# Performance work log

Measured on AMD Instinct MI355X. Metric: run time of the kernel, lower is better.

## Reference

```python
import jax, jax.numpy as jnp
import numpy as np

N_LAYER = 4
N_HEAD = 12
D_MODEL = 768
SEQ_LEN = 2048
VOCAB = 50257
BATCH = 2


def _sinusoid_pe(seq_len, d_model):
    pos = np.arange(seq_len, dtype=np.float32)[:, None]
    div = np.exp(np.arange(0, d_model, 2, dtype=np.float32) * (-np.log(10000.0) / d_model))
    pe = np.zeros((seq_len, d_model), dtype=np.float32)
    pe[:, 0::2] = np.sin(pos * div)
    pe[:, 1::2] = np.cos(pos * div)
    return jnp.asarray(pe[None])  # [1, C, D]


def setup_inputs() -> dict:
    key = jax.random.key(0)
    ks = jax.random.split(key, 12)
    s = 0.02
    return {
        "features": jax.random.randint(ks[0], (BATCH, SEQ_LEN), 0, VOCAB),
        "targets": jax.random.randint(ks[1], (BATCH, SEQ_LEN), 0, VOCAB),
        "tok_embed": jax.random.normal(ks[2], (VOCAB, D_MODEL), jnp.float32) * s,
        "pos_emb": _sinusoid_pe(SEQ_LEN, D_MODEL),
        "ln1_w": jnp.ones((N_LAYER, D_MODEL), jnp.float32),
        "ln1_b": jnp.zeros((N_LAYER, D_MODEL), jnp.float32),
        "attn_w": jax.random.normal(ks[3], (N_LAYER, D_MODEL, 3 * D_MODEL), jnp.float32) * s,
        "attn_b": jnp.zeros((N_LAYER, 3 * D_MODEL), jnp.float32),
        "proj_w": jax.random.normal(ks[4], (N_LAYER, D_MODEL, D_MODEL), jnp.float32) * s,
        "proj_b": jnp.zeros((N_LAYER, D_MODEL), jnp.float32),
        "ln2_w": jnp.ones((N_LAYER, D_MODEL), jnp.float32),
        "ln2_b": jnp.zeros((N_LAYER, D_MODEL), jnp.float32),
        "ffn_w1": jax.random.normal(ks[5], (N_LAYER, D_MODEL, 4 * D_MODEL), jnp.float32) * s,
        "ffn_b1": jnp.zeros((N_LAYER, 4 * D_MODEL), jnp.float32),
        "ffn_w2": jax.random.normal(ks[6], (N_LAYER, 4 * D_MODEL, D_MODEL), jnp.float32) * s,
        "ffn_b2": jnp.zeros((N_LAYER, D_MODEL), jnp.float32),
        "lnf_w": jnp.ones((D_MODEL,), jnp.float32),
        "lnf_b": jnp.zeros((D_MODEL,), jnp.float32),
        "final_w": jax.random.normal(ks[7], (D_MODEL, VOCAB), jnp.float32) * s,
    }


def _layernorm(x, w, b, eps=1e-5):
    mu = jnp.mean(x, axis=-1, keepdims=True)
    var = jnp.var(x, axis=-1, keepdims=True)
    return (x - mu) * jax.lax.rsqrt(var + eps) * w + b


def _attention(x, wqkv, bqkv, wo, bo):
    B, C, E = x.shape
    dh = E // N_HEAD
    qkv = x @ wqkv + bqkv  # [B, C, 3E]
    q, k, v = jnp.split(qkv, 3, axis=-1)
    q = q.reshape(B, C, N_HEAD, dh)
    k = k.reshape(B, C, N_HEAD, dh)
    v = v.reshape(B, C, N_HEAD, dh)
    att = jnp.einsum("bqhd,bkhd->bhqk", q, k) / jnp.sqrt(jnp.float32(dh))
    causal = jnp.tril(jnp.ones((C, C), bool))
    att = jnp.where(causal, att, -jnp.inf)
    att = jax.nn.softmax(att, axis=-1)
    y = jnp.einsum("bhqk,bkhd->bqhd", att, v).reshape(B, C, E)
    return y @ wo + bo


def reference(features, targets, tok_embed, pos_emb, ln1_w, ln1_b, attn_w, attn_b,
              proj_w, proj_b, ln2_w, ln2_b, ffn_w1, ffn_b1, ffn_w2, ffn_b2,
              lnf_w, lnf_b, final_w):
    C = features.shape[1]
    x = tok_embed[features] + pos_emb[:, :C]
    for l in range(N_LAYER):
        h = _layernorm(x, ln1_w[l], ln1_b[l])
        x = x + _attention(h, attn_w[l], attn_b[l], proj_w[l], proj_b[l])
        h = _layernorm(x, ln2_w[l], ln2_b[l])
        h = jax.nn.gelu(h @ ffn_w1[l] + ffn_b1[l], approximate=False) @ ffn_w2[l] + ffn_b2[l]
        x = x + h
    x = _layernorm(x, lnf_w, lnf_b)
    logits = x @ final_w  # [B, C, V]
    logp = jax.nn.log_softmax(logits, axis=-1)
    tgt = targets.reshape(-1)
    valid = tgt != -1
    tgt_safe = jnp.where(valid, tgt, 0)
    nll = -jnp.take_along_axis(logp.reshape(-1, logits.shape[-1]), tgt_safe[:, None], axis=1)[:, 0]
    loss = jnp.sum(jnp.where(valid, nll, 0.0)) / jnp.maximum(jnp.sum(valid), 1)
    return logits, loss
```

## Files before the change

kernel.cpp:

```cpp
#include <hip/hip_runtime.h>
#include <math.h>

#define N_LAYER 4
#define N_HEAD  12
#define D_MODEL 768
#define SEQ     2048
#define VOCAB   50257
#define BATCH   2
#define MROWS   (BATCH*SEQ)

typedef __bf16 bf16;
typedef __bf16 bf16x8 __attribute__((ext_vector_type(8)));
typedef float  f32x4  __attribute__((ext_vector_type(4)));
typedef short  short8v __attribute__((ext_vector_type(8)));

__device__ __forceinline__ void gload16(const bf16* g, const bf16* l) {
    __builtin_amdgcn_global_load_lds(
        (const __attribute__((address_space(1))) void*)g,
        (__attribute__((address_space(3))) void*)l,
        16, 0, 0);
}

__global__ __launch_bounds__(256) void embed_kernel(
    const int* __restrict__ feat, const float* __restrict__ tok,
    const float* __restrict__ pos, float* __restrict__ x)
{
    int row = blockIdx.x;
    int cpos = row & (SEQ - 1);
    int tid = feat[row];
    const float* te = tok + (size_t)tid * D_MODEL;
    const float* pe = pos + (size_t)cpos * D_MODEL;
    float* xr = x + (size_t)row * D_MODEL;
    for (int c = threadIdx.x; c < D_MODEL; c += 256)
        xr[c] = te[c] + pe[c];
}

__global__ __launch_bounds__(256) void ln_kernel(
    const float* __restrict__ x, const float* __restrict__ w,
    const float* __restrict__ b, bf16* __restrict__ out)
{
    int row = blockIdx.x;
    const float* xr = x + (size_t)row * D_MODEL;
    float lv[3];
    float s = 0.f, ss = 0.f;
#pragma unroll
    for (int i = 0; i < 3; i++) {
        float v = xr[threadIdx.x + i * 256];
        lv[i] = v; s += v; ss += v * v;
    }
#pragma unroll
    for (int o = 32; o; o >>= 1) { s += __shfl_down(s, o, 64); ss += __shfl_down(ss, o, 64); }
    __shared__ float red[8];
    int wid = threadIdx.x >> 6;
    if ((threadIdx.x & 63) == 0) { red[wid] = s; red[wid + 4] = ss; }
    __syncthreads();
    s  = red[0] + red[1] + red[2] + red[3];
    ss = red[4] + red[5] + red[6] + red[7];
    float mu  = s * (1.f / D_MODEL);
    float var = ss * (1.f / D_MODEL) - mu * mu;
    float rs  = rsqrtf(var + 1e-5f);
#pragma unroll
    for (int i = 0; i < 3; i++) {
        int c = threadIdx.x + i * 256;
        out[(size_t)row * D_MODEL + c] = (bf16)((lv[i] - mu) * rs * w[c] + b[c]);
    }
}

__global__ __launch_bounds__(256) void transpose_conv_kernel(
    const float* __restrict__ W, bf16* __restrict__ Wt, int K, int N)
{
    int l = blockIdx.z;
    const float* Wl = W + (size_t)l * K * N;
    bf16* Wtl = Wt + (size_t)l * K * N;
    __shared__ float tile[32][33];
    int k0 = blockIdx.y * 32, n0 = blockIdx.x * 32;
    for (int idx = threadIdx.x; idx < 1024; idx += 256) {
        int i = idx >> 5, j = idx & 31;
        int n = n0 + j;
        tile[i][j] = (n < N) ? Wl[(size_t)(k0 + i) * N + n] : 0.f;
    }
    __syncthreads();
    for (int idx = threadIdx.x; idx < 1024; idx += 256) {
        int j = idx >> 5, i = idx & 31;
        int n = n0 + j;
        if (n < N) Wtl[(size_t)n * K + k0 + i] = (bf16)tile[i][j];
    }
}

__global__ __launch_bounds__(256) void vtrans_kernel(
    const bf16* __restrict__ qkv, bf16* __restrict__ vT)
{
    int j0 = blockIdx.x * 64, h = blockIdx.y, b = blockIdx.z;
    __shared__ bf16 t[64][72];
    const bf16* src = qkv + ((size_t)b * SEQ + j0) * (3 * D_MODEL) + 2 * D_MODEL + h * 64;
    int tid = threadIdx.x;
#pragma unroll
    for (int i = 0; i < 2; i++) {
        int c = tid + i * 256;
        int j = c >> 3, d8 = (c & 7) * 8;
        *(short8v*)&t[j][d8] = *(const short8v*)&src[(size_t)j * (3 * D_MODEL) + d8];
    }
    __syncthreads();
    bf16* dst = vT + ((size_t)(b * N_HEAD + h) * 64) * SEQ;
#pragma unroll
    for (int i = 0; i < 2; i++) {
        int c = tid + i * 256;
        int d = c >> 3, j8 = (c & 7) * 8;
        bf16 tmp[8];
#pragma unroll
        for (int e = 0; e < 8; e++) tmp[e] = t[j8 + e][d];
        *(short8v*)&dst[(size_t)d * SEQ + j0 + j8] = *(const short8v*)tmp;
    }
}

template<bool BIAS, bool GELU_, int OUTM, int SPLITK>
__global__ __launch_bounds__(256) void gemm_kernel(
    const bf16* __restrict__ A, const bf16* __restrict__ Bt,
    const float* __restrict__ bias, void* __restrict__ Cout,
    int M, int N, int K)
{
    __shared__ __align__(16) bf16 As[2][128 * 32];
    __shared__ __align__(16) bf16 Bs[2][128 * 32];
    int tid = threadIdx.x;
    int lane = tid & 63, wid = tid >> 6;

    int Kslice = K / SPLITK;
    int kbase = (SPLITK > 1) ? (int)blockIdx.z * Kslice : 0;

    int row0 = blockIdx.x * 128;
    int col0 = blockIdx.y * 128;

    int wr = (wid >> 1) * 64, wc = (wid & 1) * 64;

    int srow = wid * 16 + (lane >> 2);
    int selem = (lane & 3) * 8;
    const bf16* Ab0 = A + (size_t)(row0 + srow) * K + kbase + selem;
    const bf16* Ab1 = Ab0 + (size_t)64 * K;
    int bn0 = col0 + srow;      if (bn0 >= N) bn0 = N - 1;
    int bn1 = col0 + srow + 64; if (bn1 >= N) bn1 = N - 1;
    const bf16* Bb0 = Bt + (size_t)bn0 * K + kbase + selem;
    const bf16* Bb1 = Bt + (size_t)bn1 * K + kbase + selem;

    const int nt = Kslice >> 5;
    int fr = lane & 15, fg8 = (lane >> 4) * 8;

    auto stage = [&](int t, int b) {
        int k0 = t * 32;
        gload16(Ab0 + k0, As[b] + wid * 512);
        gload16(Ab1 + k0, As[b] + (wid + 4) * 512);
        gload16(Bb0 + k0, Bs[b] + wid * 512);
        gload16(Bb1 + k0, Bs[b] + (wid + 4) * 512);
    };

    f32x4 acc[4][4] = {};
    stage(0, 0);

    for (int t = 0; t < nt; ++t) {
        int cur = t & 1;
        if (t + 1 < nt) {
            stage(t + 1, cur ^ 1);
            asm volatile("s_waitcnt vmcnt(4)" ::: "memory");
        } else {
            asm volatile("s_waitcnt vmcnt(0)" ::: "memory");
        }
        __builtin_amdgcn_s_barrier();

        bf16x8 af[4], bfr[4];
#pragma unroll
        for (int m = 0; m < 4; m++) af[m] = *(const bf16x8*)&As[cur][(wr + m * 16 + fr) * 32 + fg8];
#pragma unroll
        for (int n = 0; n < 4; n++) bfr[n] = *(const bf16x8*)&Bs[cur][(wc + n * 16 + fr) * 32 + fg8];
#pragma unroll
        for (int m = 0; m < 4; m++)
#pragma unroll
            for (int n = 0; n < 4; n++)
                acc[m][n] = __builtin_amdgcn_mfma_f32_16x16x32_bf16(af[m], bfr[n], acc[m][n], 0, 0, 0);

        asm volatile("s_waitcnt lgkmcnt(0)" ::: "memory");
        __builtin_amdgcn_s_barrier();
    }

    int g = lane >> 4;
    bool addbias = BIAS && (SPLITK == 1 || blockIdx.z == 0);

#pragma unroll
    for (int m = 0; m < 4; m++) {
#pragma unroll
        for (int n = 0; n < 4; n++) {
            int col = col0 + wc + n * 16 + fr;
            bool ok = (col < N);
            float bv = (addbias && ok) ? bias[col] : 0.f;
#pragma unroll
            for (int r = 0; r < 4; r++) {
                int row = row0 + wr + m * 16 + g * 4 + r;
                float v = acc[m][n][r] + bv;
                if (GELU_) v = 0.5f * v * (1.f + erff(v * 0.70710678118f));
                if (ok) {
                    if (OUTM == 0)
                        ((float*)Cout)[(size_t)row * N + col] = v;
                    else if (OUTM == 1)
                        ((bf16*)Cout)[(size_t)row * N + col] = (bf16)v;
                    else if (SPLITK > 1)
                        atomicAdd(&((float*)Cout)[(size_t)row * N + col], v);
                    else
                        ((float*)Cout)[(size_t)row * N + col] += v;
                }
            }
        }
    }
}

__global__ __launch_bounds__(512, 2) void gemm256_logits_kernel(
    const bf16* __restrict__ A, const bf16* __restrict__ Bt,
    float* __restrict__ Cout, float* __restrict__ rowsum, int N, int K)
{
    __shared__ __align__(16) bf16 As[2][256 * 64];
    __shared__ __align__(16) bf16 Bs[2][256 * 64];
    int tid = threadIdx.x, lane = tid & 63, wid = tid >> 6;
    int wm = wid >> 2, wn = wid & 3;
    int row0 = blockIdx.x * 256, col0 = blockIdx.y * 256;
    int fr = lane & 15, fg8 = (lane >> 4) * 8, g = lane >> 4;

    int srow_c = lane >> 3;
    int scol   = ((lane & 7) ^ srow_c) * 8;
    int sw     = (fr & 7) << 3;
    int cswz0  = (0 * 32 + fg8) ^ sw;
    int cswz1  = (1 * 32 + fg8) ^ sw;

    const int nt = K >> 6;

    auto stageA = [&](int t, int half) {
        int buf = t & 1, k0 = t * 64;
#pragma unroll
        for (int j = 0; j < 2; j++) {
            int rloc = half * 128 + (wid * 2 + j) * 8;
            gload16(A + (size_t)(row0 + rloc + srow_c) * K + k0 + scol,
                    As[buf] + rloc * 64);
        }
    };
    auto stageB = [&](int t, int half) {
        int buf = t & 1, k0 = t * 64;
#pragma unroll
        for (int j = 0; j < 2; j++) {
            int rloc = half * 128 + (wid * 2 + j) * 8;
            int grow = col0 + rloc + srow_c;
            if (grow >= N) grow = N - 1;
            gload16(Bt + (size_t)grow * K + k0 + scol,
                    Bs[buf] + rloc * 64);
        }
    };

    f32x4 acc[8][4] = {};

    stageA(0, 0); stageA(0, 1); stageB(0, 0); stageB(0, 1);
    stageB(1, 0); stageB(1, 1);
    asm volatile("s_waitcnt vmcnt(4)" ::: "memory");
    __builtin_amdgcn_s_barrier();

    for (int t = 0; t < nt; ++t) {
        int c = t & 1;
        const bf16* Ac = As[c];
        const bf16* Bc = Bs[c];

        bf16x8 bfrag[4][2];
#pragma unroll
        for (int n = 0; n < 4; n++) {
            bfrag[n][0] = *(const bf16x8*)&Bc[(wn * 64 + n * 16 + fr) * 64 + cswz0];
            bfrag[n][1] = *(const bf16x8*)&Bc[(wn * 64 + n * 16 + fr) * 64 + cswz1];
        }
        {
            bf16x8 a_[2][2];
#pragma unroll
            for (int mi = 0; mi < 2; mi++) {
                a_[mi][0] = *(const bf16x8*)&Ac[(wm * 128 + mi * 16 + fr) * 64 + cswz0];
                a_[mi][1] = *(const bf16x8*)&Ac[(wm * 128 + mi * 16 + fr) * 64 + cswz1];
            }
            if (t + 1 < nt) stageA(t + 1, 0);
            __builtin_amdgcn_s_barrier();
            __builtin_amdgcn_s_setprio(1);
#pragma unroll
            for (int mi = 0; mi < 2; mi++)
#pragma unroll
                for (int n = 0; n < 4; n++)
#pragma unroll
                    for (int ks = 0; ks < 2; ks++)
                        acc[mi][n] = __builtin_amdgcn_mfma_f32_16x16x32_bf16(a_[mi][ks], bfrag[n][ks], acc[mi][n], 0, 0, 0);
            __builtin_amdgcn_s_setprio(0);
            __builtin_amdgcn_s_barrier();
        }
        {
            bf16x8 a_[2][2];
#pragma unroll
            for (int mi = 0; mi < 2; mi++) {
                a_[mi][0] = *(const bf16x8*)&Ac[(wm * 128 + (2 + mi) * 16 + fr) * 64 + cswz0];
                a_[mi][1] = *(const bf16x8*)&Ac[(wm * 128 + (2 + mi) * 16 + fr) * 64 + cswz1];
            }
            if (t + 1 < nt) stageA(t + 1, 1);
            if (t + 2 < nt) stageB(t + 2, 0);
            __builtin_amdgcn_s_barrier();
            __builtin_amdgcn_s_setprio(1);
#pragma unroll
            for (int mi = 0; mi < 2; mi++)
#pragma unroll
                for (int n = 0; n < 4; n++)
#pragma unroll
                    for (int ks = 0; ks < 2; ks++)
                        acc[2 + mi][n] = __builtin_amdgcn_mfma_f32_16x16x32_bf16(a_[mi][ks], bfrag[n][ks], acc[2 + mi][n], 0, 0, 0);
            __builtin_amdgcn_s_setprio(0);
            __builtin_amdgcn_s_barrier();
        }
        {
            bf16x8 a_[2][2];
#pragma unroll
            for (int mi = 0; mi < 2; mi++) {
                a_[mi][0] = *(const bf16x8*)&Ac[(wm * 128 + (4 + mi) * 16 + fr) * 64 + cswz0];
                a_[mi][1] = *(const bf16x8*)&Ac[(wm * 128 + (4 + mi) * 16 + fr) * 64 + cswz1];
            }
            if (t + 2 < nt) stageB(t + 2, 1);
            __builtin_amdgcn_s_barrier();
            __builtin_amdgcn_s_setprio(1);
#pragma unroll
            for (int mi = 0; mi < 2; mi++)
#pragma unroll
                for (int n = 0; n < 4; n++)
#pragma unroll
                    for (int ks = 0; ks < 2; ks++)
                        acc[4 + mi][n] = __builtin_amdgcn_mfma_f32_16x16x32_bf16(a_[mi][ks], bfrag[n][ks], acc[4 + mi][n], 0, 0, 0);
            __builtin_amdgcn_s_setprio(0);
            __builtin_amdgcn_s_barrier();
        }
        {
            bf16x8 a_[2][2];
#pragma unroll
            for (int mi = 0; mi < 2; mi++) {
                a_[mi][0] = *(const bf16x8*)&Ac[(wm * 128 + (6 + mi) * 16 + fr) * 64 + cswz0];
                a_[mi][1] = *(const bf16x8*)&Ac[(wm * 128 + (6 + mi) * 16 + fr) * 64 + cswz1];
            }
            __builtin_amdgcn_s_barrier();
            __builtin_amdgcn_s_setprio(1);
#pragma unroll
            for (int mi = 0; mi < 2; mi++)
#pragma unroll
                for (int n = 0; n < 4; n++)
#pragma unroll
                    for (int ks = 0; ks < 2; ks++)
                        acc[6 + mi][n] = __builtin_amdgcn_mfma_f32_16x16x32_bf16(a_[mi][ks], bfrag[n][ks], acc[6 + mi][n], 0, 0, 0);
            __builtin_amdgcn_s_setprio(0);
            if (t + 2 < nt)
                asm volatile("s_waitcnt vmcnt(4)" ::: "memory");
            else if (t + 1 < nt)
                asm volatile("s_waitcnt vmcnt(0)" ::: "memory");
            __builtin_amdgcn_s_barrier();
        }
    }

#pragma unroll
    for (int mf = 0; mf < 8; mf++) {
        float lsum[4] = {0.f, 0.f, 0.f, 0.f};
#pragma unroll
        for (int n = 0; n < 4; n++) {
            int col = col0 + wn * 64 + n * 16 + fr;
            bool ok = (col < N);
#pragma unroll
            for (int r = 0; r < 4; r++) {
                int row = row0 + wm * 128 + mf * 16 + g * 4 + r;
                float v = acc[mf][n][r];
                if (ok) {
                    Cout[(size_t)row * N + col] = v;
                    lsum[r] += __expf(v);
                }
            }
        }
#pragma unroll
        for (int r = 0; r < 4; r++) {
            float s = lsum[r];
#pragma unroll
            for (int o = 1; o < 16; o <<= 1) s += __shfl_xor(s, o, 64);
            if (fr == 0)
                atomicAdd(&rowsum[row0 + wm * 128 + mf * 16 + g * 4 + r], s);
        }
    }
}

__global__ __launch_bounds__(256) void attn_kernel(
    const bf16* __restrict__ qkv, const bf16* __restrict__ vT, bf16* __restrict__ y)
{
    int qt = (int)(gridDim.x - 1 - blockIdx.x), h = blockIdx.y, b = blockIdx.z;
    const size_t rs = 3 * D_MODEL;
    int tid = threadIdx.x, lane = tid & 63, wid = tid >> 6;
    int fr = lane & 15, g = lane >> 4;
    int wq = qt * 64 + wid * 16;

    const bf16* qb = qkv + (size_t)b * SEQ * rs + h * 64;
    const bf16* kb = qb + D_MODEL;
    const bf16* vb = vT + ((size_t)(b * N_HEAD + h) * 64) * SEQ;

    __shared__ bf16 Ps[4][16][72];

    bf16x8 aq[2];
#pragma unroll
    for (int kk = 0; kk < 2; kk++)
        aq[kk] = *(const bf16x8*)&qb[(size_t)(wq + fr) * rs + kk * 32 + g * 8];

    f32x4 acco[4] = {};
    float mrow[4], lrow[4];
#pragma unroll
    for (int r = 0; r < 4; r++) { mrow[r] = -1e30f; lrow[r] = 0.f; }

    int jmax = qt * 64;
    for (int j0 = 0; j0 <= jmax; j0 += 64) {
        f32x4 accs[4] = {};
#pragma unroll
        for (int n = 0; n < 4; n++)
#pragma unroll
            for (int kk = 0; kk < 2; kk++) {
                bf16x8 bk = *(const bf16x8*)&kb[(size_t)(j0 + n * 16 + fr) * rs + kk * 32 + g * 8];
                accs[n] = __builtin_amdgcn_mfma_f32_16x16x32_bf16(aq[kk], bk, accs[n], 0, 0, 0);
            }

        bool diag = (j0 == jmax);
#pragma unroll
        for (int n = 0; n < 4; n++) {
            int jc = j0 + n * 16 + fr;
#pragma unroll
            for (int r = 0; r < 4; r++) {
                float sv = accs[n][r] * 0.125f;
                if (diag) { int irow = wq + g * 4 + r; if (jc > irow) sv = -1e30f; }
                accs[n][r] = sv;
            }
        }

        float pscale[4];
#pragma unroll
        for (int r = 0; r < 4; r++) {
            float pm = fmaxf(fmaxf(accs[0][r], accs[1][r]), fmaxf(accs[2][r], accs[3][r]));
#pragma unroll
            for (int o = 1; o < 16; o <<= 1) pm = fmaxf(pm, __shfl_xor(pm, o, 64));
            float mnew = fmaxf(mrow[r], pm);
            float corr = __expf(mrow[r] - mnew);
            mrow[r] = mnew;
            float ls = 0.f;
#pragma unroll
            for (int n = 0; n < 4; n++) {
                float p = __expf(accs[n][r] - mnew);
                accs[n][r] = p; ls += p;
            }
#pragma unroll
            for (int o = 1; o < 16; o <<= 1) ls += __shfl_xor(ls, o, 64);
            lrow[r] = lrow[r] * corr + ls;
            pscale[r] = corr;
        }
#pragma unroll
        for (int n = 0; n < 4; n++)
#pragma unroll
            for (int r = 0; r < 4; r++) acco[n][r] *= pscale[r];

#pragma unroll
        for (int n = 0; n < 4; n++)
#pragma unroll
            for (int r = 0; r < 4; r++)
                Ps[wid][g * 4 + r][n * 16 + fr] = (bf16)accs[n][r];

        bf16x8 ap[2];
#pragma unroll
        for (int kk = 0; kk < 2; kk++)
            ap[kk] = *(const bf16x8*)&Ps[wid][fr][kk * 32 + g * 8];
#pragma unroll
        for (int kk = 0; kk < 2; kk++)
#pragma unroll
            for (int n = 0; n < 4; n++) {
                bf16x8 bv = *(const bf16x8*)&vb[(size_t)(n * 16 + fr) * SEQ + j0 + kk * 32 + g * 8];
                acco[n] = __builtin_amdgcn_mfma_f32_16x16x32_bf16(ap[kk], bv, acco[n], 0, 0, 0);
            }
    }

    bf16* yb = y + (size_t)b * SEQ * D_MODEL + h * 64;
#pragma unroll
    for (int n = 0; n < 4; n++)
#pragma unroll
        for (int r = 0; r < 4; r++) {
            int row = wq + g * 4 + r;
            yb[(size_t)row * D_MODEL + n * 16 + fr] = (bf16)(acco[n][r] / lrow[r]);
        }
}

__global__ __launch_bounds__(256) void loss_nll_kernel(
    const float* __restrict__ logits, const float* __restrict__ rowsum,
    const int* __restrict__ tgt, float* __restrict__ accum)
{
    int row = blockIdx.x * 256 + threadIdx.x;
    if (row >= MROWS) return;
    int t = tgt[row];
    if (t >= 0) {
        float nll = logf(rowsum[row]) - logits[(size_t)row * VOCAB + t];
        atomicAdd(accum, nll);
        atomicAdd(accum + 1, 1.f);
    }
}

__global__ void loss_final_kernel(const float* __restrict__ accum, float* __restrict__ out)
{
    out[0] = accum[0] / fmaxf(accum[1], 1.f);
}

extern "C" void kernel_launch(void* const* d_in, const int* in_sizes, int n_in,
                              void* d_out, int out_size, void* d_ws, size_t ws_size,
                              hipStream_t stream)
{
    const int*   feat  = (const int*)d_in[0];
    const int*   tgt   = (const int*)d_in[1];
    const float* tok   = (const float*)d_in[2];
    const float* pos   = (const float*)d_in[3];
    const float* ln1w  = (const float*)d_in[4];
    const float* ln1b  = (const float*)d_in[5];
    const float* attnw = (const float*)d_in[6];
    const float* attnb = (const float*)d_in[7];
    const float* projw = (const float*)d_in[8];
    const float* projb = (const float*)d_in[9];
    const float* ln2w  = (const float*)d_in[10];
    const float* ln2b  = (const float*)d_in[11];
    const float* fw1   = (const float*)d_in[12];
    const float* fb1   = (const float*)d_in[13];
    const float* fw2   = (const float*)d_in[14];
    const float* fb2   = (const float*)d_in[15];
    const float* lnfw  = (const float*)d_in[16];
    const float* lnfb  = (const float*)d_in[17];
    const float* finw  = (const float*)d_in[18];

    char* ws = (char*)d_ws;
    size_t off = 0;
    auto alloc = [&](size_t bytes) -> void* {
        void* p = ws + off; off += (bytes + 255) & ~(size_t)255; return p;
    };
    float* x     = (float*)alloc((size_t)MROWS * D_MODEL * 4);
    bf16*  h     = (bf16*) alloc((size_t)MROWS * D_MODEL * 2);
    bf16*  big   = (bf16*) alloc((size_t)MROWS * 4 * D_MODEL * 2);
    bf16*  ybuf  = (bf16*) alloc((size_t)MROWS * D_MODEL * 2);
    bf16*  vT    = (bf16*) alloc((size_t)BATCH * N_HEAD * 64 * SEQ * 2);
    bf16*  awt   = (bf16*) alloc((size_t)N_LAYER * 3 * D_MODEL * D_MODEL * 2);
    bf16*  pwt   = (bf16*) alloc((size_t)N_LAYER * D_MODEL * D_MODEL * 2);
    bf16*  f1wt  = (bf16*) alloc((size_t)N_LAYER * 4 * D_MODEL * D_MODEL * 2);
    bf16*  f2wt  = (bf16*) alloc((size_t)N_LAYER * 4 * D_MODEL * D_MODEL * 2);
    bf16*  fwt   = (bf16*) alloc((size_t)VOCAB * D_MODEL * 2);
    float* rowsum= (float*)alloc((size_t)MROWS * 4);
    float* accum = (float*)alloc(256);

    float* logits = (float*)d_out;
    float* lossp  = (float*)d_out + (size_t)MROWS * VOCAB;

    dim3 blk(256);
    transpose_conv_kernel<<<dim3(3 * D_MODEL / 32, D_MODEL / 32, N_LAYER), blk, 0, stream>>>(attnw, awt, D_MODEL, 3 * D_MODEL);
    transpose_conv_kernel<<<dim3(D_MODEL / 32, D_MODEL / 32, N_LAYER), blk, 0, stream>>>(projw, pwt, D_MODEL, D_MODEL);
    transpose_conv_kernel<<<dim3(4 * D_MODEL / 32, D_MODEL / 32, N_LAYER), blk, 0, stream>>>(fw1, f1wt, D_MODEL, 4 * D_MODEL);
    transpose_conv_kernel<<<dim3(D_MODEL / 32, 4 * D_MODEL / 32, N_LAYER), blk, 0, stream>>>(fw2, f2wt, 4 * D_MODEL, D_MODEL);
    transpose_conv_kernel<<<dim3((VOCAB + 31) / 32, D_MODEL / 32, 1), blk, 0, stream>>>(finw, fwt, D_MODEL, VOCAB);

    embed_kernel<<<MROWS, blk, 0, stream>>>(feat, tok, pos, x);

    for (int l = 0; l < N_LAYER; l++) {
        ln_kernel<<<MROWS, blk, 0, stream>>>(x, ln1w + l * D_MODEL, ln1b + l * D_MODEL, h);
        gemm_kernel<true, false, 1, 1><<<dim3(MROWS / 128, (3 * D_MODEL) / 128), blk, 0, stream>>>(
            h, awt + (size_t)l * 3 * D_MODEL * D_MODEL, attnb + l * 3 * D_MODEL, big,
            MROWS, 3 * D_MODEL, D_MODEL);
        vtrans_kernel<<<dim3(SEQ / 64, N_HEAD, BATCH), blk, 0, stream>>>(big, vT);
        attn_kernel<<<dim3(SEQ / 64, N_HEAD, BATCH), blk, 0, stream>>>(big, vT, ybuf);
        gemm_kernel<true, false, 2, 2><<<dim3(MROWS / 128, D_MODEL / 128, 2), blk, 0, stream>>>(
            ybuf, pwt + (size_t)l * D_MODEL * D_MODEL, projb + l * D_MODEL, x,
            MROWS, D_MODEL, D_MODEL);
        ln_kernel<<<MROWS, blk, 0, stream>>>(x, ln2w + l * D_MODEL, ln2b + l * D_MODEL, h);
        gemm_kernel<true, true, 1, 1><<<dim3(MROWS / 128, (4 * D_MODEL) / 128), blk, 0, stream>>>(
            h, f1wt + (size_t)l * 4 * D_MODEL * D_MODEL, fb1 + l * 4 * D_MODEL, big,
            MROWS, 4 * D_MODEL, D_MODEL);
        gemm_kernel<true, false, 2, 2><<<dim3(MROWS / 128, D_MODEL / 128, 2), blk, 0, stream>>>(
            big, f2wt + (size_t)l * 4 * D_MODEL * D_MODEL, fb2 + l * D_MODEL, x,
            MROWS, D_MODEL, 4 * D_MODEL);
    }

    ln_kernel<<<MROWS, blk, 0, stream>>>(x, lnfw, lnfb, h);

    hipMemsetAsync(rowsum, 0, (size_t)MROWS * 4, stream);
    hipMemsetAsync(accum, 0, 8, stream);

    gemm256_logits_kernel<<<dim3(MROWS / 256, (VOCAB + 255) / 256), dim3(512), 0, stream>>>(
        h, fwt, logits, rowsum, VOCAB, D_MODEL);

    loss_nll_kernel<<<(MROWS + 255) / 256, blk, 0, stream>>>(logits, rowsum, tgt, accum);
    loss_final_kernel<<<1, 1, 0, stream>>>(accum, lossp);

    (void)in_sizes; (void)n_in; (void)out_size; (void)ws_size;
}
```

Before: 2.070 ms.

## Use BK=64 XOR-swizzled LDS tiles in the GEMM, drop split-K for proj

The generic GEMM kernel's K-step grows from 32 to 64, so each iteration now issues twice as many MFMAs per barrier pair. LDS rows use an XOR swizzle on the 8-element column chunks to avoid bank conflicts on the wider rows. The projection GEMM no longer splits K in two, which replaces its atomics with plain read-modify-write accumulates into x. The cost is doubled LDS use per block, which may lower occupancy, and fewer blocks for the projection GEMM.

```diff
diff --git a/kernel.cpp b/kernel.cpp
--- a/kernel.cpp
+++ b/kernel.cpp
@@ -119,37 +119,36 @@
     const float* __restrict__ bias, void* __restrict__ Cout,
     int M, int N, int K)
 {
-    __shared__ __align__(16) bf16 As[2][128 * 32];
-    __shared__ __align__(16) bf16 Bs[2][128 * 32];
-    int tid = threadIdx.x;
-    int lane = tid & 63, wid = tid >> 6;
+    __shared__ __align__(16) bf16 As[2][128 * 64];
+    __shared__ __align__(16) bf16 Bs[2][128 * 64];
+    int tid = threadIdx.x, lane = tid & 63, wid = tid >> 6;
 
     int Kslice = K / SPLITK;
     int kbase = (SPLITK > 1) ? (int)blockIdx.z * Kslice : 0;
 
-    int row0 = blockIdx.x * 128;
-    int col0 = blockIdx.y * 128;
-
+    int row0 = blockIdx.x * 128, col0 = blockIdx.y * 128;
     int wr = (wid >> 1) * 64, wc = (wid & 1) * 64;
-
-    int srow = wid * 16 + (lane >> 2);
-    int selem = (lane & 3) * 8;
-    const bf16* Ab0 = A + (size_t)(row0 + srow) * K + kbase + selem;
-    const bf16* Ab1 = Ab0 + (size_t)64 * K;
-    int bn0 = col0 + srow;      if (bn0 >= N) bn0 = N - 1;
-    int bn1 = col0 + srow + 64; if (bn1 >= N) bn1 = N - 1;
-    const bf16* Bb0 = Bt + (size_t)bn0 * K + kbase + selem;
-    const bf16* Bb1 = Bt + (size_t)bn1 * K + kbase + selem;
-
-    const int nt = Kslice >> 5;
-    int fr = lane & 15, fg8 = (lane >> 4) * 8;
-
-    auto stage = [&](int t, int b) {
-        int k0 = t * 32;
-        gload16(Ab0 + k0, As[b] + wid * 512);
-        gload16(Ab1 + k0, As[b] + (wid + 4) * 512);
-        gload16(Bb0 + k0, Bs[b] + wid * 512);
-        gload16(Bb1 + k0, Bs[b] + (wid + 4) * 512);
+    int fr = lane & 15, fg8 = (lane >> 4) * 8, g = lane >> 4;
+
+    int srow_c = lane >> 3;
+    int scol   = ((lane & 7) ^ srow_c) * 8;
+    int sw     = (fr & 7) << 3;
+    int cswz0  = (0 * 32 + fg8) ^ sw;
+    int cswz1  = (1 * 32 + fg8) ^ sw;
+
+    const int nt = Kslice >> 6;
+
+    auto stage = [&](int t, int buf) {
+        int k0 = kbase + t * 64;
+#pragma unroll
+        for (int j = 0; j < 4; j++) {
+            int rloc = j * 32 + wid * 8;
+            gload16(A + (size_t)(row0 + rloc + srow_c) * K + k0 + scol,
+                    As[buf] + rloc * 64);
+            int br = col0 + rloc + srow_c; if (br >= N) br = N - 1;
+            gload16(Bt + (size_t)br * K + k0 + scol,
+                    Bs[buf] + rloc * 64);
+        }
     };
 
     f32x4 acc[4][4] = {};
@@ -159,28 +158,37 @@
         int cur = t & 1;
         if (t + 1 < nt) {
             stage(t + 1, cur ^ 1);
-            asm volatile("s_waitcnt vmcnt(4)" ::: "memory");
+            asm volatile("s_waitcnt vmcnt(8)" ::: "memory");
         } else {
             asm volatile("s_waitcnt vmcnt(0)" ::: "memory");
         }
         __builtin_amdgcn_s_barrier();
 
-        bf16x8 af[4], bfr[4];
-#pragma unroll
-        for (int m = 0; m < 4; m++) af[m] = *(const bf16x8*)&As[cur][(wr + m * 16 + fr) * 32 + fg8];
-#pragma unroll
-        for (int n = 0; n < 4; n++) bfr[n] = *(const bf16x8*)&Bs[cur][(wc + n * 16 + fr) * 32 + fg8];
+        const bf16* Ac = As[cur];
+        const bf16* Bc = Bs[cur];
+        bf16x8 af[4][2], bfr[4][2];
+#pragma unroll
+        for (int m = 0; m < 4; m++) {
+            af[m][0] = *(const bf16x8*)&Ac[(wr + m * 16 + fr) * 64 + cswz0];
+            af[m][1] = *(const bf16x8*)&Ac[(wr + m * 16 + fr) * 64 + cswz1];
+        }
+#pragma unroll
+        for (int n = 0; n < 4; n++) {
+            bfr[n][0] = *(const bf16x8*)&Bc[(wc + n * 16 + fr) * 64 + cswz0];
+            bfr[n][1] = *(const bf16x8*)&Bc[(wc + n * 16 + fr) * 64 + cswz1];
+        }
 #pragma unroll
         for (int m = 0; m < 4; m++)
 #pragma unroll
             for (int n = 0; n < 4; n++)
-                acc[m][n] = __builtin_amdgcn_mfma_f32_16x16x32_bf16(af[m], bfr[n], acc[m][n], 0, 0, 0);
+#pragma unroll
+                for (int ks = 0; ks < 2; ks++)
+                    acc[m][n] = __builtin_amdgcn_mfma_f32_16x16x32_bf16(af[m][ks], bfr[n][ks], acc[m][n], 0, 0, 0);
 
         asm volatile("s_waitcnt lgkmcnt(0)" ::: "memory");
         __builtin_amdgcn_s_barrier();
     }
 
-    int g = lane >> 4;
     bool addbias = BIAS && (SPLITK == 1 || blockIdx.z == 0);
 
 #pragma unroll
@@ -196,9 +204,7 @@
                 float v = acc[m][n][r] + bv;
                 if (GELU_) v = 0.5f * v * (1.f + erff(v * 0.70710678118f));
                 if (ok) {
-                    if (OUTM == 0)
-                        ((float*)Cout)[(size_t)row * N + col] = v;
-                    else if (OUTM == 1)
+                    if (OUTM == 1)
                         ((bf16*)Cout)[(size_t)row * N + col] = (bf16)v;
                     else if (SPLITK > 1)
                         atomicAdd(&((float*)Cout)[(size_t)row * N + col], v);
@@ -564,7 +570,7 @@
             MROWS, 3 * D_MODEL, D_MODEL);
         vtrans_kernel<<<dim3(SEQ / 64, N_HEAD, BATCH), blk, 0, stream>>>(big, vT);
         attn_kernel<<<dim3(SEQ / 64, N_HEAD, BATCH), blk, 0, stream>>>(big, vT, ybuf);
-        gemm_kernel<true, false, 2, 2><<<dim3(MROWS / 128, D_MODEL / 128, 2), blk, 0, stream>>>(
+        gemm_kernel<true, false, 2, 1><<<dim3(MROWS / 128, D_MODEL / 128), blk, 0, stream>>>(
             ybuf, pwt + (size_t)l * D_MODEL * D_MODEL, projb + l * D_MODEL, x,
             MROWS, D_MODEL, D_MODEL);
         ln_kernel<<<MROWS, blk, 0, stream>>>(x, ln2w + l * D_MODEL, ln2b + l * D_MODEL, h);
```

Result: slower. 2.192 ms (+5.9%).

## Fuse V transpose into QKV GEMM epilogue and use warp-per-row layernorm

Applied to the files above, without the earlier changes.

The QKV projection GEMM epilogue now writes the V part straight into the transposed per-head vT layout, so the separate vtrans kernel launch and its extra read and write of V go away. Layernorm is changed to process one row per wavefront, four rows per block, using only shuffle reductions instead of a shared-memory reduction and __syncthreads. The cost is that the fused V stores are scattered 2-byte writes with a stride of SEQ, which coalesce poorly. The OUTM==0 path is dropped.

```diff
diff --git a/kernel.cpp b/kernel.cpp
--- a/kernel.cpp
+++ b/kernel.cpp
@@ -39,29 +39,25 @@
     const float* __restrict__ x, const float* __restrict__ w,
     const float* __restrict__ b, bf16* __restrict__ out)
 {
-    int row = blockIdx.x;
+    int wid = threadIdx.x >> 6, lane = threadIdx.x & 63;
+    int row = blockIdx.x * 4 + wid;
     const float* xr = x + (size_t)row * D_MODEL;
-    float lv[3];
+    float lv[12];
     float s = 0.f, ss = 0.f;
 #pragma unroll
-    for (int i = 0; i < 3; i++) {
-        float v = xr[threadIdx.x + i * 256];
+    for (int i = 0; i < 12; i++) {
+        float v = xr[lane + i * 64];
         lv[i] = v; s += v; ss += v * v;
     }
 #pragma unroll
     for (int o = 32; o; o >>= 1) { s += __shfl_down(s, o, 64); ss += __shfl_down(ss, o, 64); }
-    __shared__ float red[8];
-    int wid = threadIdx.x >> 6;
-    if ((threadIdx.x & 63) == 0) { red[wid] = s; red[wid + 4] = ss; }
-    __syncthreads();
-    s  = red[0] + red[1] + red[2] + red[3];
-    ss = red[4] + red[5] + red[6] + red[7];
+    s = __shfl(s, 0, 64); ss = __shfl(ss, 0, 64);
     float mu  = s * (1.f / D_MODEL);
     float var = ss * (1.f / D_MODEL) - mu * mu;
     float rs  = rsqrtf(var + 1e-5f);
 #pragma unroll
-    for (int i = 0; i < 3; i++) {
-        int c = threadIdx.x + i * 256;
+    for (int i = 0; i < 12; i++) {
+        int c = lane + i * 64;
         out[(size_t)row * D_MODEL + c] = (bf16)((lv[i] - mu) * rs * w[c] + b[c]);
     }
 }
@@ -87,36 +83,11 @@
     }
 }
 
-__global__ __launch_bounds__(256) void vtrans_kernel(
-    const bf16* __restrict__ qkv, bf16* __restrict__ vT)
-{
-    int j0 = blockIdx.x * 64, h = blockIdx.y, b = blockIdx.z;
-    __shared__ bf16 t[64][72];
-    const bf16* src = qkv + ((size_t)b * SEQ + j0) * (3 * D_MODEL) + 2 * D_MODEL + h * 64;
-    int tid = threadIdx.x;
-#pragma unroll
-    for (int i = 0; i < 2; i++) {
-        int c = tid + i * 256;
-        int j = c >> 3, d8 = (c & 7) * 8;
-        *(short8v*)&t[j][d8] = *(const short8v*)&src[(size_t)j * (3 * D_MODEL) + d8];
-    }
-    __syncthreads();
-    bf16* dst = vT + ((size_t)(b * N_HEAD + h) * 64) * SEQ;
-#pragma unroll
-    for (int i = 0; i < 2; i++) {
-        int c = tid + i * 256;
-        int d = c >> 3, j8 = (c & 7) * 8;
-        bf16 tmp[8];
-#pragma unroll
-        for (int e = 0; e < 8; e++) tmp[e] = t[j8 + e][d];
-        *(short8v*)&dst[(size_t)d * SEQ + j0 + j8] = *(const short8v*)tmp;
-    }
-}
-
 template<bool BIAS, bool GELU_, int OUTM, int SPLITK>
 __global__ __launch_bounds__(256) void gemm_kernel(
     const bf16* __restrict__ A, const bf16* __restrict__ Bt,
     const float* __restrict__ bias, void* __restrict__ Cout,
+    bf16* __restrict__ vTout,
     int M, int N, int K)
 {
     __shared__ __align__(16) bf16 As[2][128 * 32];
@@ -196,10 +167,18 @@
                 float v = acc[m][n][r] + bv;
                 if (GELU_) v = 0.5f * v * (1.f + erff(v * 0.70710678118f));
                 if (ok) {
-                    if (OUTM == 0)
-                        ((float*)Cout)[(size_t)row * N + col] = v;
-                    else if (OUTM == 1)
+                    if (OUTM == 1)
                         ((bf16*)Cout)[(size_t)row * N + col] = (bf16)v;
+                    else if (OUTM == 3) {
+                        if (col < 2 * D_MODEL) {
+                            ((bf16*)Cout)[(size_t)row * N + col] = (bf16)v;
+                        } else {
+                            int c2 = col - 2 * D_MODEL;
+                            int hh = c2 >> 6, dd = c2 & 63;
+                            int bb = row >> 11, ss = row & (SEQ - 1);
+                            vTout[(((size_t)(bb * N_HEAD + hh) * 64 + dd) << 11) + ss] = (bf16)v;
+                        }
+                    }
                     else if (SPLITK > 1)
                         atomicAdd(&((float*)Cout)[(size_t)row * N + col], v);
                     else
@@ -558,25 +537,24 @@
     embed_kernel<<<MROWS, blk, 0, stream>>>(feat, tok, pos, x);
 
     for (int l = 0; l < N_LAYER; l++) {
-        ln_kernel<<<MROWS, blk, 0, stream>>>(x, ln1w + l * D_MODEL, ln1b + l * D_MODEL, h);
-        gemm_kernel<true, false, 1, 1><<<dim3(MROWS / 128, (3 * D_MODEL) / 128), blk, 0, stream>>>(
-            h, awt + (size_t)l * 3 * D_MODEL * D_MODEL, attnb + l * 3 * D_MODEL, big,
+        ln_kernel<<<MROWS / 4, blk, 0, stream>>>(x, ln1w + l * D_MODEL, ln1b + l * D_MODEL, h);
+        gemm_kernel<true, false, 3, 1><<<dim3(MROWS / 128, (3 * D_MODEL) / 128), blk, 0, stream>>>(
+            h, awt + (size_t)l * 3 * D_MODEL * D_MODEL, attnb + l * 3 * D_MODEL, big, vT,
             MROWS, 3 * D_MODEL, D_MODEL);
-        vtrans_kernel<<<dim3(SEQ / 64, N_HEAD, BATCH), blk, 0, stream>>>(big, vT);
         attn_kernel<<<dim3(SEQ / 64, N_HEAD, BATCH), blk, 0, stream>>>(big, vT, ybuf);
         gemm_kernel<true, false, 2, 2><<<dim3(MROWS / 128, D_MODEL / 128, 2), blk, 0, stream>>>(
-            ybuf, pwt + (size_t)l * D_MODEL * D_MODEL, projb + l * D_MODEL, x,
+            ybuf, pwt + (size_t)l * D_MODEL * D_MODEL, projb + l * D_MODEL, x, nullptr,
             MROWS, D_MODEL, D_MODEL);
-        ln_kernel<<<MROWS, blk, 0, stream>>>(x, ln2w + l * D_MODEL, ln2b + l * D_MODEL, h);
+        ln_kernel<<<MROWS / 4, blk, 0, stream>>>(x, ln2w + l * D_MODEL, ln2b + l * D_MODEL, h);
         gemm_kernel<true, true, 1, 1><<<dim3(MROWS / 128, (4 * D_MODEL) / 128), blk, 0, stream>>>(
-            h, f1wt + (size_t)l * 4 * D_MODEL * D_MODEL, fb1 + l * 4 * D_MODEL, big,
+            h, f1wt + (size_t)l * 4 * D_MODEL * D_MODEL, fb1 + l * 4 * D_MODEL, big, nullptr,
             MROWS, 4 * D_MODEL, D_MODEL);
         gemm_kernel<true, false, 2, 2><<<dim3(MROWS / 128, D_MODEL / 128, 2), blk, 0, stream>>>(
-            big, f2wt + (size_t)l * 4 * D_MODEL * D_MODEL, fb2 + l * D_MODEL, x,
+            big, f2wt + (size_t)l * 4 * D_MODEL * D_MODEL, fb2 + l * D_MODEL, x, nullptr,
             MROWS, D_MODEL, 4 * D_MODEL);
     }
 
-    ln_kernel<<<MROWS, blk, 0, stream>>>(x, lnfw, lnfb, h);
+    ln_kernel<<<MROWS / 4, blk, 0, stream>>>(x, lnfw, lnfb, h);
 
     hipMemsetAsync(rowsum, 0, (size_t)MROWS * 4, stream);
     hipMemsetAsync(accum, 0, 8, stream);
```

New measurement: 2.069 ms (median of 2 runs). No clear change (-0.0%).
